# Kernel optimization log

Measured on AMD Instinct MI355X. Metric: run time of the kernel, lower is better.

Reference implementation:

```python
import jax, jax.numpy as jnp
import numpy as np

N_NODES = 50000
N_EDGES = 800000
HIDDEN = 128
NUM_GDL = 2


def setup_inputs() -> dict:
    key = jax.random.key(0)
    k0, k1, k2, k3, k4 = jax.random.split(key, 5)
    x = jax.random.normal(k0, (N_NODES, HIDDEN), dtype=jnp.float32)
    row = jax.random.randint(k1, (N_EDGES,), 0, N_NODES, dtype=jnp.int32)
    # ensure every node appears at least once as a target so degree >= 1
    col_tail = jax.random.randint(k2, (N_EDGES - N_NODES,), 0, N_NODES, dtype=jnp.int32)
    col = jnp.concatenate([jnp.arange(N_NODES, dtype=jnp.int32), col_tail])
    edge_index = jnp.stack([row, col], axis=0)  # [2, E]
    W1s = jax.random.normal(k3, (NUM_GDL, HIDDEN, HIDDEN), dtype=jnp.float32) / np.sqrt(HIDDEN).astype(np.float32)
    W2s = jax.random.normal(k4, (NUM_GDL, HIDDEN, 2 * HIDDEN), dtype=jnp.float32) / np.sqrt(2 * HIDDEN).astype(np.float32)
    biases = jnp.zeros((NUM_GDL, HIDDEN), dtype=jnp.float32)  # reset_parameters zeroes bias
    return {"x": x, "edge_index": edge_index, "W1s": W1s, "W2s": W2s, "biases": biases}


def reference(x, edge_index, W1s, W2s, biases):
    # eval mode: dropout is identity
    row, col = edge_index[0], edge_index[1]  # row = source j, col = target i
    n, d = x.shape
    deg = jax.ops.segment_sum(jnp.ones(row.shape[0], x.dtype), col, num_segments=n)
    norm = (1.0 / deg)[row]  # per-edge norm, indexed by row as in torch source
    for k in range(W1s.shape[0]):
        W1, W2, b = W1s[k], W2s[k], biases[k]
        # lin2(cat[x_i, x_j]) = x_i @ W2[:, :d].T + x_j @ W2[:, d:].T
        # precompute both node-level projections, then gather per edge (cheaper than per-edge GEMM)
        proj_i = x @ W2[:, :d].T  # [n, d]
        proj_j = x @ W2[:, d:].T  # [n, d]
        msg = norm[:, None] * (proj_i[col] + proj_j[row])  # [E, d]
        agg = jax.ops.segment_sum(msg, col, num_segments=n)  # scatter-add into targets
        out = x @ W1.T - agg + b
        x = jax.nn.gelu(out, approximate=False)  # torch nn.GELU default = exact erf
    return x
```

## Files before the change

### kernel.cpp

```cpp
#include <hip/hip_runtime.h>

#define N_NODES 50000
#define N_EDGES 800000
#define D 128
#define NBUCKET 196
#define CAP 8192
#define EPT 16
#define SCAT_BLOCKS 196
#define WCONV_BLOCKS 96
#define CAST_BLOCKS 6250
#define GEMM_TILES 391

typedef unsigned short ushort_t;
typedef __bf16 bf16x8 __attribute__((ext_vector_type(8)));
typedef float f32x4 __attribute__((ext_vector_type(4)));

__device__ __forceinline__ ushort_t f2bf(float f) {
    unsigned u = __builtin_bit_cast(unsigned, f);
    u += 0x7FFFu + ((u >> 16) & 1u);
    return (ushort_t)(u >> 16);
}
__device__ __forceinline__ float bf2f(unsigned h16) {
    return __builtin_bit_cast(float, h16 << 16);
}

__global__ __launch_bounds__(256) void k_pre(const float* __restrict__ x, ushort_t* __restrict__ xb,
                                             const int* __restrict__ row, const int* __restrict__ col,
                                             int* __restrict__ bucket_cursor, int2* __restrict__ temp,
                                             const float* __restrict__ W1s, const float* __restrict__ W2s,
                                             ushort_t* __restrict__ Wb) {
    __shared__ int hist[NBUCKET];
    int b = blockIdx.x;
    if (b < SCAT_BLOCKS) {
        for (int t = threadIdx.x; t < NBUCKET; t += 256) hist[t] = 0;
        __syncthreads();
        int base = (b * 256 + threadIdx.x) * EPT;
        bool act = base < N_EDGES;
        int4 c[4], r[4];
        if (act) {
            #pragma unroll
            for (int q = 0; q < 4; ++q) c[q] = *(const int4*)(col + base + q * 4);
            #pragma unroll
            for (int q = 0; q < 4; ++q) r[q] = *(const int4*)(row + base + q * 4);
            #pragma unroll
            for (int q = 0; q < 4; ++q) {
                atomicAdd(&hist[c[q].x >> 8], 1); atomicAdd(&hist[c[q].y >> 8], 1);
                atomicAdd(&hist[c[q].z >> 8], 1); atomicAdd(&hist[c[q].w >> 8], 1);
            }
        }
        __syncthreads();
        for (int t = threadIdx.x; t < NBUCKET; t += 256) {
            int cnt = hist[t];
            hist[t] = cnt ? atomicAdd(&bucket_cursor[t], cnt) : 0;
        }
        __syncthreads();
        if (act) {
            #pragma unroll
            for (int q = 0; q < 4; ++q) {
                int cc[4] = { c[q].x, c[q].y, c[q].z, c[q].w };
                int rr[4] = { r[q].x, r[q].y, r[q].z, r[q].w };
                #pragma unroll
                for (int e = 0; e < 4; ++e) {
                    int bk = cc[e] >> 8;
                    int pos = atomicAdd(&hist[bk], 1);
                    temp[bk * CAP + pos] = make_int2(rr[e], cc[e]);
                }
            }
        }
    } else if (b < SCAT_BLOCKS + WCONV_BLOCKS) {
        int c = (b - SCAT_BLOCKS) * 256 + threadIdx.x;
        int k = c / 12288, rem = c % 12288;
        int mat = rem / 4096, rr = (rem % 4096) / 32, col4 = rem % 32;
        const float* src = (mat == 0)
            ? (W1s + k * 16384 + rr * 128 + col4 * 4)
            : (W2s + k * 32768 + rr * 256 + (mat == 2 ? 128 : 0) + col4 * 4);
        float4 v = *(const float4*)src;
        ushort_t tmp[4] = { f2bf(v.x), f2bf(v.y), f2bf(v.z), f2bf(v.w) };
        *(uint2*)(Wb + ((size_t)(k * 3 + mat)) * 16384 + rr * 128 + col4 * 4) = *(const uint2*)tmp;
    } else {
        int base = ((b - SCAT_BLOCKS - WCONV_BLOCKS) * 256 + threadIdx.x) * 4;
        if (base < N_NODES * D) {
            float4 v = *(const float4*)(x + base);
            ushort_t tmp[4] = { f2bf(v.x), f2bf(v.y), f2bf(v.z), f2bf(v.w) };
            *(uint2*)(xb + base) = *(const uint2*)tmp;
        }
    }
}

__device__ __forceinline__ void gemm_tile3(int m0,
                                           ushort_t (*As)[136], ushort_t (*Bs)[136],
                                           const ushort_t* __restrict__ xb,
                                           const ushort_t* __restrict__ Wl,
                                           ushort_t* __restrict__ Plb,
                                           ushort_t* __restrict__ Pi_,
                                           ushort_t* __restrict__ Pj) {
    const int tid = threadIdx.x;
    #pragma unroll
    for (int it = 0; it < 8; ++it) {
        int c = tid + it * 256;
        int r = c >> 4, kc = c & 15;
        uint4 v = make_uint4(0, 0, 0, 0);
        int gm = m0 + r;
        if (gm < N_NODES) v = *(const uint4*)(xb + (size_t)gm * D + kc * 8);
        *(uint4*)&As[r][kc * 8] = v;
    }
    const int w = tid >> 6, lane = tid & 63, quad = lane >> 4, r16 = lane & 15;
    const int arow0 = w * 32 + r16, arow1 = arow0 + 16;
    #pragma unroll
    for (int y = 0; y < 3; ++y) {
        const ushort_t* Wmat = Wl + (size_t)y * 16384;
        #pragma unroll
        for (int it = 0; it < 8; ++it) {
            int c = tid + it * 256;
            int r = c >> 4, kc = c & 15;
            *(uint4*)&Bs[r][kc * 8] = *(const uint4*)(Wmat + r * 128 + kc * 8);
        }
        __syncthreads();
        f32x4 acc[2][8];
        #pragma unroll
        for (int mt = 0; mt < 2; ++mt)
            #pragma unroll
            for (int nt = 0; nt < 8; ++nt) acc[mt][nt] = (f32x4){0.f, 0.f, 0.f, 0.f};
        #pragma unroll
        for (int k0 = 0; k0 < 128; k0 += 32) {
            bf16x8 a0 = __builtin_bit_cast(bf16x8, *(const uint4*)&As[arow0][k0 + quad * 8]);
            bf16x8 a1 = __builtin_bit_cast(bf16x8, *(const uint4*)&As[arow1][k0 + quad * 8]);
            #pragma unroll
            for (int nt = 0; nt < 8; ++nt) {
                bf16x8 b = __builtin_bit_cast(bf16x8, *(const uint4*)&Bs[nt * 16 + r16][k0 + quad * 8]);
                acc[0][nt] = __builtin_amdgcn_mfma_f32_16x16x32_bf16(b, a0, acc[0][nt], 0, 0, 0);
                acc[1][nt] = __builtin_amdgcn_mfma_f32_16x16x32_bf16(b, a1, acc[1][nt], 0, 0, 0);
            }
        }
        ushort_t* Outp = (y == 0) ? Plb : (y == 1 ? Pi_ : Pj);
        #pragma unroll
        for (int mt = 0; mt < 2; ++mt) {
            int gm = m0 + w * 32 + mt * 16 + r16;
            if (gm >= N_NODES) continue;
            #pragma unroll
            for (int nt = 0; nt < 8; ++nt) {
                ushort_t tmp[4] = { f2bf(acc[mt][nt][0]), f2bf(acc[mt][nt][1]),
                                    f2bf(acc[mt][nt][2]), f2bf(acc[mt][nt][3]) };
                *(uint2*)(Outp + (size_t)gm * D + nt * 16 + quad * 4) = *(const uint2*)tmp;
            }
        }
        if (y < 2) __syncthreads();
    }
}

__global__ __launch_bounds__(256) void k_bsort_gemm(const int2* __restrict__ temp,
                                                    const int* __restrict__ bucket_cursor,
                                                    int* __restrict__ csr, int* __restrict__ off,
                                                    int* __restrict__ deg, float* __restrict__ inv_deg,
                                                    const ushort_t* __restrict__ xb,
                                                    const ushort_t* __restrict__ Wb,
                                                    ushort_t* __restrict__ Plb,
                                                    ushort_t* __restrict__ Pi_,
                                                    ushort_t* __restrict__ Pj) {
    __shared__ __align__(16) ushort_t As[128][136];
    __shared__ __align__(16) ushort_t Bs[128][136];
    __shared__ int hist[256];
    __shared__ int sm[256];
    if (blockIdx.x < NBUCKET) {
        int b = blockIdx.x, t = threadIdx.x;
        int cnt = bucket_cursor[b];
        sm[t] = (t < b) ? bucket_cursor[t] : 0;
        __syncthreads();
        for (int o = 1; o < 256; o <<= 1) {
            int add = (t >= o) ? sm[t - o] : 0;
            __syncthreads();
            sm[t] += add;
            __syncthreads();
        }
        int gbase = sm[255];
        int tbase = b * CAP;
        hist[t] = 0;
        __syncthreads();
        int i = t;
        for (; i + 768 < cnt; i += 1024) {
            int2 e0 = temp[tbase + i], e1 = temp[tbase + i + 256];
            int2 e2 = temp[tbase + i + 512], e3 = temp[tbase + i + 768];
            atomicAdd(&hist[e0.y & 255], 1); atomicAdd(&hist[e1.y & 255], 1);
            atomicAdd(&hist[e2.y & 255], 1); atomicAdd(&hist[e3.y & 255], 1);
        }
        for (; i < cnt; i += 256) atomicAdd(&hist[temp[tbase + i].y & 255], 1);
        __syncthreads();
        int c = hist[t];
        sm[t] = c;
        __syncthreads();
        for (int o = 1; o < 256; o <<= 1) {
            int add = (t >= o) ? sm[t - o] : 0;
            __syncthreads();
            sm[t] += add;
            __syncthreads();
        }
        int excl = sm[t] - c;
        int node = b * 256 + t;
        if (node < N_NODES) {
            off[node] = gbase + excl;
            deg[node] = c;
            inv_deg[node] = 1.0f / (float)c;
        }
        __syncthreads();
        hist[t] = gbase + excl;
        __syncthreads();
        i = t;
        for (; i + 768 < cnt; i += 1024) {
            int2 e0 = temp[tbase + i], e1 = temp[tbase + i + 256];
            int2 e2 = temp[tbase + i + 512], e3 = temp[tbase + i + 768];
            int p0 = atomicAdd(&hist[e0.y & 255], 1);
            int p1 = atomicAdd(&hist[e1.y & 255], 1);
            int p2 = atomicAdd(&hist[e2.y & 255], 1);
            int p3 = atomicAdd(&hist[e3.y & 255], 1);
            csr[p0] = e0.x; csr[p1] = e1.x; csr[p2] = e2.x; csr[p3] = e3.x;
        }
        for (; i < cnt; i += 256) {
            int2 e = temp[tbase + i];
            int p = atomicAdd(&hist[e.y & 255], 1);
            csr[p] = e.x;
        }
    } else {
        gemm_tile3((blockIdx.x - NBUCKET) * 128, As, Bs, xb, Wb, Plb, Pi_, Pj);
    }
}

__global__ __launch_bounds__(256) void k_gemm(const ushort_t* __restrict__ xb,
                                              const ushort_t* __restrict__ Wl,
                                              ushort_t* __restrict__ Plb,
                                              ushort_t* __restrict__ Pi_,
                                              ushort_t* __restrict__ Pj) {
    __shared__ __align__(16) ushort_t As[128][136];
    __shared__ __align__(16) ushort_t Bs[128][136];
    gemm_tile3(blockIdx.x * 128, As, Bs, xb, Wl, Plb, Pi_, Pj);
}

__global__ __launch_bounds__(256) void k_agg(const ushort_t* __restrict__ Plb,
                                             const ushort_t* __restrict__ Pi_,
                                             const ushort_t* __restrict__ Pj,
                                             const int* __restrict__ off,
                                             const int* __restrict__ deg,
                                             const int* __restrict__ csr,
                                             const float* __restrict__ inv_deg,
                                             const float* __restrict__ bias,
                                             float* __restrict__ out_f32,
                                             ushort_t* __restrict__ out_bf16,
                                             int write_bf16) {
    int wv = __builtin_amdgcn_readfirstlane(threadIdx.x >> 6);
    int node = blockIdx.x * 4 + wv;
    int lane = threadIdx.x & 63;
    if (node >= N_NODES) return;
    unsigned ulin = *(const unsigned*)(Plb + (size_t)node * D + 2 * lane);
    unsigned upi  = *(const unsigned*)(Pi_ + (size_t)node * D + 2 * lane);
    float2 bv = *(const float2*)(bias + 2 * lane);
    float a0 = bf2f(ulin & 0xffffu) + bv.x;
    float a1 = bf2f(ulin >> 16)     + bv.y;
    float c0 = 0.f, c1 = 0.f, si = 0.f, sj = 0.f;
    int e0 = off[node], ne = deg[node];
    int j = 0;
    for (; j + 16 <= ne; j += 16) {
        int sx[16];
        #pragma unroll
        for (int t = 0; t < 16; ++t) sx[t] = csr[e0 + j + t];
        unsigned p[16];
        #pragma unroll
        for (int t = 0; t < 16; ++t) p[t] = *(const unsigned*)(Pj + (size_t)sx[t] * D + 2 * lane);
        float dv[16];
        #pragma unroll
        for (int t = 0; t < 16; ++t) dv[t] = inv_deg[sx[t]];
        #pragma unroll
        for (int t = 0; t < 16; t += 2) {
            si += dv[t];
            sj += dv[t + 1];
            a0 -= dv[t] * bf2f(p[t] & 0xffffu) + dv[t + 1] * bf2f(p[t + 1] & 0xffffu);
            a1 -= dv[t] * bf2f(p[t] >> 16)     + dv[t + 1] * bf2f(p[t + 1] >> 16);
        }
    }
    for (; j + 4 <= ne; j += 4) {
        int s0 = csr[e0 + j], s1 = csr[e0 + j + 1], s2 = csr[e0 + j + 2], s3 = csr[e0 + j + 3];
        unsigned p0 = *(const unsigned*)(Pj + (size_t)s0 * D + 2 * lane);
        unsigned p1 = *(const unsigned*)(Pj + (size_t)s1 * D + 2 * lane);
        unsigned p2 = *(const unsigned*)(Pj + (size_t)s2 * D + 2 * lane);
        unsigned p3 = *(const unsigned*)(Pj + (size_t)s3 * D + 2 * lane);
        float d0 = inv_deg[s0], d1 = inv_deg[s1], d2 = inv_deg[s2], d3 = inv_deg[s3];
        si += d0 + d2; sj += d1 + d3;
        a0 -= d0 * bf2f(p0 & 0xffffu) + d1 * bf2f(p1 & 0xffffu);
        a1 -= d0 * bf2f(p0 >> 16)     + d1 * bf2f(p1 >> 16);
        c0 += d2 * bf2f(p2 & 0xffffu) + d3 * bf2f(p3 & 0xffffu);
        c1 += d2 * bf2f(p2 >> 16)     + d3 * bf2f(p3 >> 16);
    }
    for (; j < ne; ++j) {
        int s0 = csr[e0 + j];
        unsigned p0 = *(const unsigned*)(Pj + (size_t)s0 * D + 2 * lane);
        float d0 = inv_deg[s0];
        si += d0;
        a0 -= d0 * bf2f(p0 & 0xffffu);
        a1 -= d0 * bf2f(p0 >> 16);
    }
    si += sj;
    a0 -= c0 + si * bf2f(upi & 0xffffu);
    a1 -= c1 + si * bf2f(upi >> 16);
    float g0 = 0.5f * a0 * (1.0f + erff(a0 * 0.70710678118654752440f));
    float g1 = 0.5f * a1 * (1.0f + erff(a1 * 0.70710678118654752440f));
    if (write_bf16) {
        ushort_t tmp[2] = { f2bf(g0), f2bf(g1) };
        *(unsigned*)(out_bf16 + (size_t)node * D + 2 * lane) = *(const unsigned*)tmp;
    } else {
        *(float2*)(out_f32 + (size_t)node * D + 2 * lane) = make_float2(g0, g1);
    }
}

extern "C" void kernel_launch(void* const* d_in, const int* in_sizes, int n_in,
                              void* d_out, int out_size, void* d_ws, size_t ws_size,
                              hipStream_t stream) {
    const float* x      = (const float*)d_in[0];
    const int*   ei     = (const int*)d_in[1];
    const int*   rowp   = ei;
    const int*   colp   = ei + N_EDGES;
    const float* W1s    = (const float*)d_in[2];
    const float* W2s    = (const float*)d_in[3];
    const float* biases = (const float*)d_in[4];
    float* out = (float*)d_out;

    char* ws = (char*)d_ws;
    size_t o = 0;
    auto carve = [&](size_t bytes) -> void* {
        void* p = ws + o;
        o = (o + bytes + 255) & ~(size_t)255;
        return p;
    };
    int*      bucket_cursor = (int*)carve(NBUCKET * 4);
    int*      deg     = (int*)carve(N_NODES * 4);
    float*    inv_deg = (float*)carve(N_NODES * 4);
    int*      off     = (int*)carve(N_NODES * 4);
    int*      csr     = (int*)carve(N_EDGES * 4);
    int2*     temp    = (int2*)carve((size_t)NBUCKET * CAP * 8);
    ushort_t* xb      = (ushort_t*)carve((size_t)N_NODES * D * 2);
    ushort_t* Wb      = (ushort_t*)carve((size_t)2 * 3 * 16384 * 2);
    ushort_t* Plb     = (ushort_t*)carve((size_t)N_NODES * D * 2);
    ushort_t* Pi_     = (ushort_t*)carve((size_t)N_NODES * D * 2);
    ushort_t* Pj      = (ushort_t*)carve((size_t)N_NODES * D * 2);
    if (o > ws_size) return;

    hipMemsetAsync(bucket_cursor, 0, NBUCKET * 4, stream);

    k_pre<<<SCAT_BLOCKS + WCONV_BLOCKS + CAST_BLOCKS, 256, 0, stream>>>(x, xb, rowp, colp,
                                                                        bucket_cursor, temp,
                                                                        W1s, W2s, Wb);
    k_bsort_gemm<<<NBUCKET + GEMM_TILES, 256, 0, stream>>>(temp, bucket_cursor, csr, off,
                                                           deg, inv_deg, xb, Wb, Plb, Pi_, Pj);

    const int AB = (N_NODES + 3) / 4;
    k_agg<<<AB, 256, 0, stream>>>(Plb, Pi_, Pj, off, deg, csr, inv_deg, biases,
                                  nullptr, xb, 1);
    k_gemm<<<GEMM_TILES, 256, 0, stream>>>(xb, Wb + (size_t)3 * 16384, Plb, Pi_, Pj);
    k_agg<<<AB, 256, 0, stream>>>(Plb, Pi_, Pj, off, deg, csr, inv_deg, biases + 128,
                                  out, nullptr, 0);
}
```

Measured before the change: 216.9 us.

## Store gathered neighbor projection in FP8 and prescale by inverse degree

The per-edge gathered projection Pj is now stored as FP8 (one byte per element) instead of bf16, which halves the bytes of the dominant random gather traffic in the aggregation kernels. In the second layer the GEMM multiplies Pj by inv_deg before the FP8 conversion, so the aggregation loop drops the per-edge inv_deg load and multiply. The per-node sum of inv_deg computed in layer 0 is saved to a new array and reused in layer 1. FP8 quantisation of the messages loses precision and may push results past the tolerance.

```diff
diff --git a/kernel.cpp b/kernel.cpp
--- a/kernel.cpp
+++ b/kernel.cpp
@@ -14,6 +14,7 @@
 typedef unsigned short ushort_t;
 typedef __bf16 bf16x8 __attribute__((ext_vector_type(8)));
 typedef float f32x4 __attribute__((ext_vector_type(4)));
+typedef float f32x2 __attribute__((ext_vector_type(2)));
 
 __device__ __forceinline__ ushort_t f2bf(float f) {
     unsigned u = __builtin_bit_cast(unsigned, f);
@@ -91,9 +92,10 @@
                                            ushort_t (*As)[136], ushort_t (*Bs)[136],
                                            const ushort_t* __restrict__ xb,
                                            const ushort_t* __restrict__ Wl,
+                                           const float* __restrict__ scl,
                                            ushort_t* __restrict__ Plb,
                                            ushort_t* __restrict__ Pi_,
-                                           ushort_t* __restrict__ Pj) {
+                                           unsigned char* __restrict__ Pj8) {
     const int tid = threadIdx.x;
     #pragma unroll
     for (int it = 0; it < 8; ++it) {
@@ -132,16 +134,26 @@
                 acc[1][nt] = __builtin_amdgcn_mfma_f32_16x16x32_bf16(b, a1, acc[1][nt], 0, 0, 0);
             }
         }
-        ushort_t* Outp = (y == 0) ? Plb : (y == 1 ? Pi_ : Pj);
         #pragma unroll
         for (int mt = 0; mt < 2; ++mt) {
             int gm = m0 + w * 32 + mt * 16 + r16;
             if (gm >= N_NODES) continue;
-            #pragma unroll
-            for (int nt = 0; nt < 8; ++nt) {
-                ushort_t tmp[4] = { f2bf(acc[mt][nt][0]), f2bf(acc[mt][nt][1]),
-                                    f2bf(acc[mt][nt][2]), f2bf(acc[mt][nt][3]) };
-                *(uint2*)(Outp + (size_t)gm * D + nt * 16 + quad * 4) = *(const uint2*)tmp;
+            if (y < 2) {
+                ushort_t* Outp = (y == 0) ? Plb : Pi_;
+                #pragma unroll
+                for (int nt = 0; nt < 8; ++nt) {
+                    ushort_t tmp[4] = { f2bf(acc[mt][nt][0]), f2bf(acc[mt][nt][1]),
+                                        f2bf(acc[mt][nt][2]), f2bf(acc[mt][nt][3]) };
+                    *(uint2*)(Outp + (size_t)gm * D + nt * 16 + quad * 4) = *(const uint2*)tmp;
+                }
+            } else {
+                float sc = scl ? scl[gm] : 1.0f;
+                #pragma unroll
+                for (int nt = 0; nt < 8; ++nt) {
+                    int v = __builtin_amdgcn_cvt_pk_fp8_f32(acc[mt][nt][0] * sc, acc[mt][nt][1] * sc, 0, false);
+                    v = __builtin_amdgcn_cvt_pk_fp8_f32(acc[mt][nt][2] * sc, acc[mt][nt][3] * sc, v, true);
+                    *(unsigned*)(Pj8 + (size_t)gm * D + nt * 16 + quad * 4) = (unsigned)v;
+                }
             }
         }
         if (y < 2) __syncthreads();
@@ -156,7 +168,7 @@
                                                     const ushort_t* __restrict__ Wb,
                                                     ushort_t* __restrict__ Plb,
                                                     ushort_t* __restrict__ Pi_,
-                                                    ushort_t* __restrict__ Pj) {
+                                                    unsigned char* __restrict__ Pj8) {
     __shared__ __align__(16) ushort_t As[128][136];
     __shared__ __align__(16) ushort_t Bs[128][136];
     __shared__ int hist[256];
@@ -220,88 +232,135 @@
             csr[p] = e.x;
         }
     } else {
-        gemm_tile3((blockIdx.x - NBUCKET) * 128, As, Bs, xb, Wb, Plb, Pi_, Pj);
+        gemm_tile3((blockIdx.x - NBUCKET) * 128, As, Bs, xb, Wb, nullptr, Plb, Pi_, Pj8);
     }
 }
 
 __global__ __launch_bounds__(256) void k_gemm(const ushort_t* __restrict__ xb,
                                               const ushort_t* __restrict__ Wl,
+                                              const float* __restrict__ inv_deg,
                                               ushort_t* __restrict__ Plb,
                                               ushort_t* __restrict__ Pi_,
-                                              ushort_t* __restrict__ Pj) {
+                                              unsigned char* __restrict__ Pj8) {
     __shared__ __align__(16) ushort_t As[128][136];
     __shared__ __align__(16) ushort_t Bs[128][136];
-    gemm_tile3(blockIdx.x * 128, As, Bs, xb, Wl, Plb, Pi_, Pj);
+    gemm_tile3(blockIdx.x * 128, As, Bs, xb, Wl, inv_deg, Plb, Pi_, Pj8);
 }
 
 __global__ __launch_bounds__(256) void k_agg(const ushort_t* __restrict__ Plb,
                                              const ushort_t* __restrict__ Pi_,
-                                             const ushort_t* __restrict__ Pj,
+                                             const unsigned char* __restrict__ Pj8,
                                              const int* __restrict__ off,
                                              const int* __restrict__ deg,
                                              const int* __restrict__ csr,
                                              const float* __restrict__ inv_deg,
                                              const float* __restrict__ bias,
+                                             float* __restrict__ s_arr,
                                              float* __restrict__ out_f32,
                                              ushort_t* __restrict__ out_bf16,
-                                             int write_bf16) {
+                                             int layer0) {
     int wv = __builtin_amdgcn_readfirstlane(threadIdx.x >> 6);
     int node = blockIdx.x * 4 + wv;
+    if (node >= N_NODES) return;
     int lane = threadIdx.x & 63;
-    if (node >= N_NODES) return;
     unsigned ulin = *(const unsigned*)(Plb + (size_t)node * D + 2 * lane);
     unsigned upi  = *(const unsigned*)(Pi_ + (size_t)node * D + 2 * lane);
     float2 bv = *(const float2*)(bias + 2 * lane);
     float a0 = bf2f(ulin & 0xffffu) + bv.x;
     float a1 = bf2f(ulin >> 16)     + bv.y;
-    float c0 = 0.f, c1 = 0.f, si = 0.f, sj = 0.f;
+    float c0 = 0.f, c1 = 0.f, si;
     int e0 = off[node], ne = deg[node];
     int j = 0;
-    for (; j + 16 <= ne; j += 16) {
-        int sx[16];
-        #pragma unroll
-        for (int t = 0; t < 16; ++t) sx[t] = csr[e0 + j + t];
-        unsigned p[16];
-        #pragma unroll
-        for (int t = 0; t < 16; ++t) p[t] = *(const unsigned*)(Pj + (size_t)sx[t] * D + 2 * lane);
-        float dv[16];
-        #pragma unroll
-        for (int t = 0; t < 16; ++t) dv[t] = inv_deg[sx[t]];
-        #pragma unroll
-        for (int t = 0; t < 16; t += 2) {
-            si += dv[t];
-            sj += dv[t + 1];
-            a0 -= dv[t] * bf2f(p[t] & 0xffffu) + dv[t + 1] * bf2f(p[t + 1] & 0xffffu);
-            a1 -= dv[t] * bf2f(p[t] >> 16)     + dv[t + 1] * bf2f(p[t + 1] >> 16);
-        }
-    }
-    for (; j + 4 <= ne; j += 4) {
-        int s0 = csr[e0 + j], s1 = csr[e0 + j + 1], s2 = csr[e0 + j + 2], s3 = csr[e0 + j + 3];
-        unsigned p0 = *(const unsigned*)(Pj + (size_t)s0 * D + 2 * lane);
-        unsigned p1 = *(const unsigned*)(Pj + (size_t)s1 * D + 2 * lane);
-        unsigned p2 = *(const unsigned*)(Pj + (size_t)s2 * D + 2 * lane);
-        unsigned p3 = *(const unsigned*)(Pj + (size_t)s3 * D + 2 * lane);
-        float d0 = inv_deg[s0], d1 = inv_deg[s1], d2 = inv_deg[s2], d3 = inv_deg[s3];
-        si += d0 + d2; sj += d1 + d3;
-        a0 -= d0 * bf2f(p0 & 0xffffu) + d1 * bf2f(p1 & 0xffffu);
-        a1 -= d0 * bf2f(p0 >> 16)     + d1 * bf2f(p1 >> 16);
-        c0 += d2 * bf2f(p2 & 0xffffu) + d3 * bf2f(p3 & 0xffffu);
-        c1 += d2 * bf2f(p2 >> 16)     + d3 * bf2f(p3 >> 16);
-    }
-    for (; j < ne; ++j) {
-        int s0 = csr[e0 + j];
-        unsigned p0 = *(const unsigned*)(Pj + (size_t)s0 * D + 2 * lane);
-        float d0 = inv_deg[s0];
-        si += d0;
-        a0 -= d0 * bf2f(p0 & 0xffffu);
-        a1 -= d0 * bf2f(p0 >> 16);
-    }
-    si += sj;
+    if (layer0) {
+        float sa = 0.f, sb = 0.f;
+        for (; j + 16 <= ne; j += 16) {
+            int sx[16];
+            #pragma unroll
+            for (int t = 0; t < 16; ++t) sx[t] = csr[e0 + j + t];
+            unsigned u[16];
+            #pragma unroll
+            for (int t = 0; t < 16; ++t) u[t] = *(const ushort_t*)(Pj8 + (size_t)sx[t] * D + 2 * lane);
+            float dv[16];
+            #pragma unroll
+            for (int t = 0; t < 16; ++t) dv[t] = inv_deg[sx[t]];
+            #pragma unroll
+            for (int t = 0; t < 16; t += 2) {
+                f32x2 f0 = __builtin_amdgcn_cvt_pk_f32_fp8((int)u[t], false);
+                f32x2 f1 = __builtin_amdgcn_cvt_pk_f32_fp8((int)u[t + 1], false);
+                sa += dv[t]; sb += dv[t + 1];
+                a0 -= dv[t] * f0[0];  c0 += dv[t + 1] * f1[0];
+                a1 -= dv[t] * f0[1];  c1 += dv[t + 1] * f1[1];
+            }
+        }
+        for (; j + 4 <= ne; j += 4) {
+            int s0 = csr[e0 + j], s1 = csr[e0 + j + 1], s2 = csr[e0 + j + 2], s3 = csr[e0 + j + 3];
+            unsigned u0 = *(const ushort_t*)(Pj8 + (size_t)s0 * D + 2 * lane);
+            unsigned u1 = *(const ushort_t*)(Pj8 + (size_t)s1 * D + 2 * lane);
+            unsigned u2 = *(const ushort_t*)(Pj8 + (size_t)s2 * D + 2 * lane);
+            unsigned u3 = *(const ushort_t*)(Pj8 + (size_t)s3 * D + 2 * lane);
+            float d0 = inv_deg[s0], d1 = inv_deg[s1], d2 = inv_deg[s2], d3 = inv_deg[s3];
+            f32x2 f0 = __builtin_amdgcn_cvt_pk_f32_fp8((int)u0, false);
+            f32x2 f1 = __builtin_amdgcn_cvt_pk_f32_fp8((int)u1, false);
+            f32x2 f2 = __builtin_amdgcn_cvt_pk_f32_fp8((int)u2, false);
+            f32x2 f3 = __builtin_amdgcn_cvt_pk_f32_fp8((int)u3, false);
+            sa += d0 + d2; sb += d1 + d3;
+            a0 -= d0 * f0[0] + d1 * f1[0];  c0 += d2 * f2[0] + d3 * f3[0];
+            a1 -= d0 * f0[1] + d1 * f1[1];  c1 += d2 * f2[1] + d3 * f3[1];
+        }
+        for (; j < ne; ++j) {
+            int s0 = csr[e0 + j];
+            unsigned u0 = *(const ushort_t*)(Pj8 + (size_t)s0 * D + 2 * lane);
+            float d0 = inv_deg[s0];
+            f32x2 f0 = __builtin_amdgcn_cvt_pk_f32_fp8((int)u0, false);
+            sa += d0;
+            a0 -= d0 * f0[0];
+            a1 -= d0 * f0[1];
+        }
+        si = sa + sb;
+        if (lane == 0) s_arr[node] = si;
+    } else {
+        si = s_arr[node];
+        for (; j + 16 <= ne; j += 16) {
+            int sx[16];
+            #pragma unroll
+            for (int t = 0; t < 16; ++t) sx[t] = csr[e0 + j + t];
+            unsigned u[16];
+            #pragma unroll
+            for (int t = 0; t < 16; ++t) u[t] = *(const ushort_t*)(Pj8 + (size_t)sx[t] * D + 2 * lane);
+            #pragma unroll
+            for (int t = 0; t < 16; t += 2) {
+                f32x2 f0 = __builtin_amdgcn_cvt_pk_f32_fp8((int)u[t], false);
+                f32x2 f1 = __builtin_amdgcn_cvt_pk_f32_fp8((int)u[t + 1], false);
+                a0 -= f0[0];  c0 += f1[0];
+                a1 -= f0[1];  c1 += f1[1];
+            }
+        }
+        for (; j + 4 <= ne; j += 4) {
+            int s0 = csr[e0 + j], s1 = csr[e0 + j + 1], s2 = csr[e0 + j + 2], s3 = csr[e0 + j + 3];
+            unsigned u0 = *(const ushort_t*)(Pj8 + (size_t)s0 * D + 2 * lane);
+            unsigned u1 = *(const ushort_t*)(Pj8 + (size_t)s1 * D + 2 * lane);
+            unsigned u2 = *(const ushort_t*)(Pj8 + (size_t)s2 * D + 2 * lane);
+            unsigned u3 = *(const ushort_t*)(Pj8 + (size_t)s3 * D + 2 * lane);
+            f32x2 f0 = __builtin_amdgcn_cvt_pk_f32_fp8((int)u0, false);
+            f32x2 f1 = __builtin_amdgcn_cvt_pk_f32_fp8((int)u1, false);
+            f32x2 f2 = __builtin_amdgcn_cvt_pk_f32_fp8((int)u2, false);
+            f32x2 f3 = __builtin_amdgcn_cvt_pk_f32_fp8((int)u3, false);
+            a0 -= f0[0] + f1[0];  c0 += f2[0] + f3[0];
+            a1 -= f0[1] + f1[1];  c1 += f2[1] + f3[1];
+        }
+        for (; j < ne; ++j) {
+            int s0 = csr[e0 + j];
+            unsigned u0 = *(const ushort_t*)(Pj8 + (size_t)s0 * D + 2 * lane);
+            f32x2 f0 = __builtin_amdgcn_cvt_pk_f32_fp8((int)u0, false);
+            a0 -= f0[0];
+            a1 -= f0[1];
+        }
+    }
     a0 -= c0 + si * bf2f(upi & 0xffffu);
     a1 -= c1 + si * bf2f(upi >> 16);
     float g0 = 0.5f * a0 * (1.0f + erff(a0 * 0.70710678118654752440f));
     float g1 = 0.5f * a1 * (1.0f + erff(a1 * 0.70710678118654752440f));
-    if (write_bf16) {
+    if (layer0) {
         ushort_t tmp[2] = { f2bf(g0), f2bf(g1) };
         *(unsigned*)(out_bf16 + (size_t)node * D + 2 * lane) = *(const unsigned*)tmp;
     } else {
@@ -328,17 +387,18 @@
         o = (o + bytes + 255) & ~(size_t)255;
         return p;
     };
-    int*      bucket_cursor = (int*)carve(NBUCKET * 4);
-    int*      deg     = (int*)carve(N_NODES * 4);
-    float*    inv_deg = (float*)carve(N_NODES * 4);
-    int*      off     = (int*)carve(N_NODES * 4);
-    int*      csr     = (int*)carve(N_EDGES * 4);
-    int2*     temp    = (int2*)carve((size_t)NBUCKET * CAP * 8);
-    ushort_t* xb      = (ushort_t*)carve((size_t)N_NODES * D * 2);
-    ushort_t* Wb      = (ushort_t*)carve((size_t)2 * 3 * 16384 * 2);
-    ushort_t* Plb     = (ushort_t*)carve((size_t)N_NODES * D * 2);
-    ushort_t* Pi_     = (ushort_t*)carve((size_t)N_NODES * D * 2);
-    ushort_t* Pj      = (ushort_t*)carve((size_t)N_NODES * D * 2);
+    int*           bucket_cursor = (int*)carve(NBUCKET * 4);
+    int*           deg     = (int*)carve(N_NODES * 4);
+    float*         inv_deg = (float*)carve(N_NODES * 4);
+    int*           off     = (int*)carve(N_NODES * 4);
+    float*         s_arr   = (float*)carve(N_NODES * 4);
+    int*           csr     = (int*)carve(N_EDGES * 4);
+    int2*          temp    = (int2*)carve((size_t)NBUCKET * CAP * 8);
+    ushort_t*      xb      = (ushort_t*)carve((size_t)N_NODES * D * 2);
+    ushort_t*      Wb      = (ushort_t*)carve((size_t)2 * 3 * 16384 * 2);
+    ushort_t*      Plb     = (ushort_t*)carve((size_t)N_NODES * D * 2);
+    ushort_t*      Pi_     = (ushort_t*)carve((size_t)N_NODES * D * 2);
+    unsigned char* Pj8     = (unsigned char*)carve((size_t)N_NODES * D);
     if (o > ws_size) return;
 
     hipMemsetAsync(bucket_cursor, 0, NBUCKET * 4, stream);
@@ -347,12 +407,12 @@
                                                                         bucket_cursor, temp,
                                                                         W1s, W2s, Wb);
     k_bsort_gemm<<<NBUCKET + GEMM_TILES, 256, 0, stream>>>(temp, bucket_cursor, csr, off,
-                                                           deg, inv_deg, xb, Wb, Plb, Pi_, Pj);
+                                                           deg, inv_deg, xb, Wb, Plb, Pi_, Pj8);
 
     const int AB = (N_NODES + 3) / 4;
-    k_agg<<<AB, 256, 0, stream>>>(Plb, Pi_, Pj, off, deg, csr, inv_deg, biases,
+    k_agg<<<AB, 256, 0, stream>>>(Plb, Pi_, Pj8, off, deg, csr, inv_deg, biases, s_arr,
                                   nullptr, xb, 1);
-    k_gemm<<<GEMM_TILES, 256, 0, stream>>>(xb, Wb + (size_t)3 * 16384, Plb, Pi_, Pj);
-    k_agg<<<AB, 256, 0, stream>>>(Plb, Pi_, Pj, off, deg, csr, inv_deg, biases + 128,
+    k_gemm<<<GEMM_TILES, 256, 0, stream>>>(xb, Wb + (size_t)3 * 16384, inv_deg, Plb, Pi_, Pj8);
+    k_agg<<<AB, 256, 0, stream>>>(Plb, Pi_, Pj8, off, deg, csr, inv_deg, biases + 128, s_arr,
                                   out, nullptr, 0);
 }
```

Result: faster. 207.5 us (-4.3%).
